# Performance work log

Measured on AMD Instinct MI355X. Metric: run time of the kernel, lower is better.

The kernel has to match this reference:

```python
import jax, jax.numpy as jnp
import numpy as np

H = 16  # n_heads
EPS = 1e-12  # F.normalize eps


def _l2norm(x):
    n = jnp.sqrt(jnp.sum(x * x, axis=-1, keepdims=True))
    return x / jnp.maximum(n, EPS)


def setup_inputs() -> dict:
    key = jax.random.key(0)
    ks = jax.random.split(key, 10)
    bs, S, dim = 2, 2048, 2048
    dh = dim // H
    x = jax.random.normal(ks[0], (bs, S, dim), dtype=jnp.float32)
    mask = jnp.ones((bs, S, S), dtype=jnp.int32)  # mask==0 would be masked out
    s = 0.02
    Wq = jax.random.normal(ks[1], (dim, dim), jnp.float32) * s
    bq = jax.random.normal(ks[2], (dim,), jnp.float32) * s
    Wk = jax.random.normal(ks[3], (dim, dim), jnp.float32) * s
    bk = jax.random.normal(ks[4], (dim,), jnp.float32) * s
    Wv = jax.random.normal(ks[5], (dim, dim), jnp.float32) * s
    bv = jax.random.normal(ks[6], (dim,), jnp.float32) * s
    Wo = jax.random.normal(ks[7], (dim, dim), jnp.float32) * s
    bo = jax.random.normal(ks[8], (dim,), jnp.float32) * s
    attention_scale = jnp.asarray(1.0 / np.sqrt(dh), dtype=jnp.float32)
    return {"x": x, "mask": mask, "Wq": Wq, "bq": bq, "Wk": Wk, "bk": bk,
            "Wv": Wv, "bv": bv, "Wo": Wo, "bo": bo,
            "attention_scale": attention_scale}


def reference(x, mask, Wq, bq, Wk, bk, Wv, bv, Wo, bo, attention_scale):
    bs, S, dim = x.shape
    dh = dim // H

    def split_heads(t):  # [bs,S,dim] -> [bs,H,S,dh]
        return t.reshape(bs, S, H, dh).transpose(0, 2, 1, 3)

    q = split_heads(x @ Wq.T + bq)
    k = split_heads(x @ Wk.T + bk)
    v = split_heads(x @ Wv.T + bv)

    # normalized attention: L2-normalize q,k then learned scale on q
    q = _l2norm(q) * attention_scale
    k = _l2norm(k)

    scores = jnp.einsum('bhqd,bhkd->bhqk', q, k)
    masked = mask[:, None, :, :] == 0  # broadcast over heads
    scores = jnp.where(masked, -jnp.inf, scores)
    weights = jax.nn.softmax(scores.astype(jnp.float32), axis=-1).astype(scores.dtype)
    # dropout p=0.0 -> identity
    ctx = jnp.einsum('bhqk,bhkd->bhqd', weights, v)
    ctx = ctx.transpose(0, 2, 1, 3).reshape(bs, S, dim)
    return ctx @ Wo.T + bo
```

## Files before the change

kernel.cpp:

```cpp
#include <hip/hip_runtime.h>
#include <stdint.h>

typedef __attribute__((ext_vector_type(8))) short short8;
typedef __attribute__((ext_vector_type(4))) float f32x4;
typedef __attribute__((ext_vector_type(4))) unsigned short ushort4v;
typedef __attribute__((ext_vector_type(4))) float float4v;
typedef __attribute__((ext_vector_type(4))) int int4v;

#define GLL16(gp, lp)                                                        \
  __builtin_amdgcn_global_load_lds(                                          \
      (const __attribute__((address_space(1))) void*)(gp),                   \
      (__attribute__((address_space(3))) void*)(lp), 16, 0, 0)

__device__ __forceinline__ unsigned short f2bf(float f) {
  union { float f; unsigned u; } v; v.f = f;
  unsigned r = v.u + 0x7FFFu + ((v.u >> 16) & 1u);
  return (unsigned short)(r >> 16);
}
__device__ __forceinline__ float bf2f(unsigned short h) {
  union { unsigned u; float f; } v; v.u = ((unsigned)h) << 16;
  return v.f;
}

__global__ __launch_bounds__(256) void cast_kernel(
    const float* __restrict__ x, const float* __restrict__ Wq,
    const float* __restrict__ Wk, const float* __restrict__ Wv,
    const float* __restrict__ Wo, const float* __restrict__ bq,
    const float* __restrict__ bk, const float* __restrict__ bv,
    unsigned short* __restrict__ xb, unsigned short* __restrict__ wqkv,
    unsigned short* __restrict__ wob, float* __restrict__ biasq) {
  const int X4 = 2097152, W4 = 1048576;
  const int total = X4 + 4 * W4 + 1536;
  for (int i = blockIdx.x * 256 + threadIdx.x; i < total; i += gridDim.x * 256) {
    if (i < X4 + 4 * W4) {
      const float* src; unsigned short* dst;
      if (i < X4) { src = x + (size_t)i * 4; dst = xb + (size_t)i * 4; }
      else {
        int j = i - X4;
        if (j < 3 * W4) {
          const float* w = (j < W4) ? Wq : (j < 2 * W4 ? Wk : Wv);
          int j0 = (j < W4) ? j : (j < 2 * W4 ? j - W4 : j - 2 * W4);
          src = w + (size_t)j0 * 4; dst = wqkv + (size_t)j * 4;
        } else {
          int j0 = j - 3 * W4; src = Wo + (size_t)j0 * 4; dst = wob + (size_t)j0 * 4;
        }
      }
      float4v v = *(const float4v*)src;
      ushort4v o; o.x = f2bf(v.x); o.y = f2bf(v.y); o.z = f2bf(v.z); o.w = f2bf(v.w);
      *(ushort4v*)dst = o;
    } else {
      int j = i - (X4 + 4 * W4);
      const float* src = (j < 512) ? bq + j * 4
                        : (j < 1024 ? bk + (j - 512) * 4 : bv + (j - 1024) * 4);
      *(float4v*)(biasq + j * 4) = *(const float4v*)src;
    }
  }
}

__global__ __launch_bounds__(256) void maskflag_kernel(const int* __restrict__ mask,
                                                       int* __restrict__ flags) {
  const int bid = blockIdx.x;
  const int b = bid >> 10, rem = bid & 1023, qt = rem >> 5, kt = rem & 31;
  const int t = threadIdx.x;
  const int* mb = mask + (size_t)b * 4194304;
  int ok = 1;
#pragma unroll
  for (int j = 0; j < 4; ++j) {
    int flat = t * 16 + j * 4;
    int r = flat >> 6, c = flat & 63;
    int4v v = *(const int4v*)(mb + (size_t)(qt * 64 + r) * 2048 + kt * 64 + c);
    ok &= (v.x != 0) & (v.y != 0) & (v.z != 0) & (v.w != 0);
  }
  int all = __syncthreads_and(ok);
  if (t == 0) flags[bid] = all;
}

template <bool OUT_BF16>
__global__ __launch_bounds__(256) void gemm_bt(
    const unsigned short* __restrict__ A, const unsigned short* __restrict__ B,
    void* __restrict__ C, const float* __restrict__ bias, int N, int K) {
  __shared__ unsigned short As[128 * 64];
  __shared__ unsigned short Bs[128 * 64];
  const int tid = threadIdx.x, lane = tid & 63;
  const int wid = __builtin_amdgcn_readfirstlane(tid >> 6);
  const int wr = wid >> 1, wc = wid & 1;
  const int bm = blockIdx.y, bn = blockIdx.x;
  const int g = lane >> 4, q15 = lane & 15;
  f32x4 acc[4][4];
#pragma unroll
  for (int i = 0; i < 4; ++i)
#pragma unroll
    for (int j = 0; j < 4; ++j) acc[i][j] = f32x4{0.f, 0.f, 0.f, 0.f};
  const size_t ldab = (size_t)K * 2;
  const int nkt = K >> 6;
  for (int kt = 0; kt < nkt; ++kt) {
#pragma unroll
    for (int i = 0; i < 4; ++i) {
      int c = i * 4 + wid;
      int o = c * 1024 + lane * 16;
      int row = o >> 7, colb = o & 127;
      GLL16((const char*)A + (size_t)(bm * 128 + row) * ldab + kt * 128 + colb,
            (char*)As + c * 1024);
      GLL16((const char*)B + (size_t)(bn * 128 + row) * ldab + kt * 128 + colb,
            (char*)Bs + c * 1024);
    }
    __syncthreads();
#pragma unroll
    for (int kk = 0; kk < 2; ++kk) {
      short8 af[4], bfv[4];
#pragma unroll
      for (int mf = 0; mf < 4; ++mf)
        af[mf] = *(const short8*)((const char*)As +
                 (wr * 64 + mf * 16 + q15) * 128 + kk * 64 + g * 16);
#pragma unroll
      for (int nf = 0; nf < 4; ++nf)
        bfv[nf] = *(const short8*)((const char*)Bs +
                  (wc * 64 + nf * 16 + q15) * 128 + kk * 64 + g * 16);
#pragma unroll
      for (int mf = 0; mf < 4; ++mf)
#pragma unroll
        for (int nf = 0; nf < 4; ++nf)
          acc[mf][nf] = __builtin_amdgcn_mfma_f32_16x16x32_bf16(
              af[mf], bfv[nf], acc[mf][nf], 0, 0, 0);
    }
    __syncthreads();
  }
#pragma unroll
  for (int nf = 0; nf < 4; ++nf) {
    int col = bn * 128 + wc * 64 + nf * 16 + q15;
    float bv = bias[col];
#pragma unroll
    for (int mf = 0; mf < 4; ++mf) {
#pragma unroll
      for (int r = 0; r < 4; ++r) {
        int row = bm * 128 + wr * 64 + mf * 16 + g * 4 + r;
        float v = acc[mf][nf][r] + bv;
        if (OUT_BF16)
          ((unsigned short*)C)[(size_t)row * N + col] = f2bf(v);
        else
          ((float*)C)[(size_t)row * N + col] = v;
      }
    }
  }
}

__global__ __launch_bounds__(256) void norm_vt_kernel(
    unsigned short* __restrict__ QKV, unsigned short* __restrict__ VT,
    const float* __restrict__ scale_p) {
  __shared__ unsigned short vt[128 * 72];
  const int bid = blockIdx.x;
  const int b = bid >> 9, h = (bid >> 5) & 15, st = bid & 31;
  const int t = threadIdx.x;
  const int r = t >> 2, qd = t & 3;
  const float scale = scale_p[0];
  unsigned short* rowp = QKV + (size_t)(b * 2048 + st * 64 + r) * 6144;
#pragma unroll
  for (int part = 0; part < 2; ++part) {
    unsigned short* p = rowp + part * 2048 + h * 128 + qd * 32;
    short8 v[4];
    float ss = 0.f;
#pragma unroll
    for (int j = 0; j < 4; ++j) {
      v[j] = *(const short8*)(p + j * 8);
#pragma unroll
      for (int e = 0; e < 8; ++e) {
        float f = bf2f((unsigned short)v[j][e]);
        ss += f * f;
      }
    }
    ss += __shfl_xor(ss, 1, 64);
    ss += __shfl_xor(ss, 2, 64);
    float inv = 1.0f / fmaxf(sqrtf(ss), 1e-12f);
    if (part == 0) inv *= scale;
#pragma unroll
    for (int j = 0; j < 4; ++j) {
      short8 w;
#pragma unroll
      for (int e = 0; e < 8; ++e)
        w[e] = (short)f2bf(bf2f((unsigned short)v[j][e]) * inv);
      *(short8*)(p + j * 8) = w;
    }
  }
  {
    const unsigned short* p = rowp + 4096 + h * 128 + qd * 32;
#pragma unroll
    for (int j = 0; j < 4; ++j) {
      short8 v = *(const short8*)(p + j * 8);
#pragma unroll
      for (int e = 0; e < 8; ++e) {
        int d = qd * 32 + j * 8 + e;
        vt[d * 72 + r] = (unsigned short)v[e];
      }
    }
  }
  __syncthreads();
  {
    const int d = t >> 1, half = t & 1;
    unsigned short* dst = VT + ((size_t)(b * 16 + h) * 128 + d) * 2048 + st * 64 + half * 32;
#pragma unroll
    for (int j = 0; j < 4; ++j)
      *(short8*)(dst + j * 8) = *(const short8*)(&vt[d * 72 + half * 32 + j * 8]);
  }
}

__global__ __launch_bounds__(256) void flash_kernel(
    const unsigned short* __restrict__ QKV, const unsigned short* __restrict__ VT,
    const int* __restrict__ flags, const int* __restrict__ mask,
    unsigned short* __restrict__ ctx) {
  __shared__ unsigned short Ks[64 * 128];
  __shared__ unsigned short Vs[128 * 64];
  __shared__ unsigned short Ps[4 * 16 * 64];
  const int tid = threadIdx.x, lane = tid & 63;
  const int wid = __builtin_amdgcn_readfirstlane(tid >> 6);
  const int g = lane >> 4, q15 = lane & 15;
  const int bid = blockIdx.x;
  const int b = bid >> 9, h = (bid >> 5) & 15, qt = bid & 31;

  short8 qf[4];
  {
    const char* qbase = (const char*)QKV +
        (size_t)(b * 2048 + qt * 64 + wid * 16 + q15) * 12288 + h * 256;
#pragma unroll
    for (int kk = 0; kk < 4; ++kk)
      qf[kk] = *(const short8*)(qbase + kk * 64 + g * 16);
  }
  f32x4 o[8];
#pragma unroll
  for (int i = 0; i < 8; ++i) o[i] = f32x4{0.f, 0.f, 0.f, 0.f};
  float mrun[4] = {-__builtin_inff(), -__builtin_inff(), -__builtin_inff(), -__builtin_inff()};
  float lrun[4] = {0.f, 0.f, 0.f, 0.f};
  char* PsW = (char*)Ps + wid * 2048;

  for (int kt = 0; kt < 32; ++kt) {
#pragma unroll
    for (int i = 0; i < 8; ++i) {
      int c = i * 4 + wid;
      if (c < 16) {
        int off = c * 1024 + lane * 16;
        int row = off >> 8, colb = off & 255;
        int scol = colb ^ ((row & 7) << 4);
        GLL16((const char*)QKV + (size_t)(b * 2048 + kt * 64 + row) * 12288 +
                  4096 + h * 256 + scol,
              (char*)Ks + c * 1024);
      } else {
        int c2 = c - 16;
        int off = c2 * 1024 + lane * 16;
        int d = off >> 7, colb = off & 127;
        int scol = colb ^ ((d & 7) << 4);
        GLL16((const char*)VT + ((size_t)(b * 16 + h) * 128 + d) * 4096 +
                  kt * 128 + scol,
              (char*)Vs + c2 * 1024);
      }
    }
    __syncthreads();

    f32x4 s[4];
#pragma unroll
    for (int nf = 0; nf < 4; ++nf) s[nf] = f32x4{0.f, 0.f, 0.f, 0.f};
#pragma unroll
    for (int nf = 0; nf < 4; ++nf) {
      int key = nf * 16 + q15;
      const char* kb = (const char*)Ks + key * 256;
      int sw = (key & 7) << 4;
#pragma unroll
      for (int kk = 0; kk < 4; ++kk) {
        short8 kf = *(const short8*)(kb + ((kk * 64 + g * 16) ^ sw));
        s[nf] = __builtin_amdgcn_mfma_f32_16x16x32_bf16(qf[kk], kf, s[nf], 0, 0, 0);
      }
    }

    if (flags[b * 1024 + qt * 32 + kt] == 0) {
#pragma unroll
      for (int nf = 0; nf < 4; ++nf)
#pragma unroll
        for (int r = 0; r < 4; ++r) {
          int q = qt * 64 + wid * 16 + g * 4 + r;
          int k = kt * 64 + nf * 16 + q15;
          if (mask[(size_t)b * 4194304 + (size_t)q * 2048 + k] == 0)
            s[nf][r] = -__builtin_inff();
        }
    }

    float rmax[4];
#pragma unroll
    for (int r = 0; r < 4; ++r)
      rmax[r] = fmaxf(fmaxf(s[0][r], s[1][r]), fmaxf(s[2][r], s[3][r]));
#pragma unroll
    for (int st = 1; st < 16; st <<= 1)
#pragma unroll
      for (int r = 0; r < 4; ++r)
        rmax[r] = fmaxf(rmax[r], __shfl_xor(rmax[r], st, 64));
    float sc_[4];
#pragma unroll
    for (int r = 0; r < 4; ++r) {
      float mn = fmaxf(mrun[r], rmax[r]);
      sc_[r] = __expf(mrun[r] - mn);
      mrun[r] = mn;
      lrun[r] *= sc_[r];
    }
#pragma unroll
    for (int d0 = 0; d0 < 8; ++d0)
#pragma unroll
      for (int r = 0; r < 4; ++r) o[d0][r] *= sc_[r];
    float rs[4] = {0.f, 0.f, 0.f, 0.f};
#pragma unroll
    for (int nf = 0; nf < 4; ++nf)
#pragma unroll
      for (int r = 0; r < 4; ++r) {
        float p = __expf(s[nf][r] - mrun[r]);
        s[nf][r] = p;
        rs[r] += p;
      }
#pragma unroll
    for (int st = 1; st < 16; st <<= 1)
#pragma unroll
      for (int r = 0; r < 4; ++r) rs[r] += __shfl_xor(rs[r], st, 64);
#pragma unroll
    for (int r = 0; r < 4; ++r) lrun[r] += rs[r];

#pragma unroll
    for (int nf = 0; nf < 4; ++nf)
#pragma unroll
      for (int r = 0; r < 4; ++r) {
        int qq = g * 4 + r;
        int kcol = nf * 16 + q15;
        int addr = qq * 128 + ((2 * kcol) ^ ((g & 3) << 4));
        *(unsigned short*)(PsW + addr) = f2bf(s[nf][r]);
      }

#pragma unroll
    for (int kk2 = 0; kk2 < 2; ++kk2) {
      short8 pf = *(const short8*)(PsW + q15 * 128 +
                   ((kk2 * 64 + g * 16) ^ (((q15 >> 2) & 3) << 4)));
#pragma unroll
      for (int d0 = 0; d0 < 8; ++d0) {
        int d = d0 * 16 + q15;
        short8 vf = *(const short8*)((const char*)Vs + d * 128 +
                     ((kk2 * 64 + g * 16) ^ ((d & 7) << 4)));
        o[d0] = __builtin_amdgcn_mfma_f32_16x16x32_bf16(pf, vf, o[d0], 0, 0, 0);
      }
    }
    __syncthreads();
  }

  float inv[4];
#pragma unroll
  for (int r = 0; r < 4; ++r) inv[r] = 1.0f / lrun[r];
#pragma unroll
  for (int d0 = 0; d0 < 8; ++d0)
#pragma unroll
    for (int r = 0; r < 4; ++r) {
      int row = b * 2048 + qt * 64 + wid * 16 + g * 4 + r;
      int col = h * 128 + d0 * 16 + q15;
      ctx[(size_t)row * 2048 + col] = f2bf(o[d0][r] * inv[r]);
    }
}

extern "C" void kernel_launch(void* const* d_in, const int* in_sizes, int n_in,
                              void* d_out, int out_size, void* d_ws, size_t ws_size,
                              hipStream_t stream) {
  const float* x  = (const float*)d_in[0];
  const int* mask = (const int*)d_in[1];
  const float* Wq = (const float*)d_in[2];
  const float* bq = (const float*)d_in[3];
  const float* Wk = (const float*)d_in[4];
  const float* bk = (const float*)d_in[5];
  const float* Wv = (const float*)d_in[6];
  const float* bv = (const float*)d_in[7];
  const float* Wo = (const float*)d_in[8];
  const float* bo = (const float*)d_in[9];
  const float* asc = (const float*)d_in[10];

  char* ws = (char*)d_ws;
  unsigned short* xb   = (unsigned short*)(ws);
  unsigned short* wqkv = (unsigned short*)(ws + ((size_t)16 << 20));
  unsigned short* wob  = (unsigned short*)(ws + ((size_t)40 << 20));
  float* biasq         = (float*)(ws + ((size_t)48 << 20));
  int* flags           = (int*)(ws + ((size_t)48 << 20) + (64 << 10));
  unsigned short* qkv  = (unsigned short*)(ws + ((size_t)49 << 20));
  unsigned short* VT   = wqkv;
  unsigned short* ctx  = xb;
  float* out = (float*)d_out;

  hipLaunchKernelGGL(cast_kernel, dim3(2048), dim3(256), 0, stream,
                     x, Wq, Wk, Wv, Wo, bq, bk, bv, xb, wqkv, wob, biasq);
  hipLaunchKernelGGL(maskflag_kernel, dim3(2048), dim3(256), 0, stream, mask, flags);
  hipLaunchKernelGGL((gemm_bt<true>), dim3(48, 32), dim3(256), 0, stream,
                     xb, wqkv, (void*)qkv, biasq, 6144, 2048);
  hipLaunchKernelGGL(norm_vt_kernel, dim3(1024), dim3(256), 0, stream, qkv, VT, asc);
  hipLaunchKernelGGL(flash_kernel, dim3(1024), dim3(256), 0, stream,
                     qkv, VT, flags, mask, ctx);
  hipLaunchKernelGGL((gemm_bt<false>), dim3(16, 32), dim3(256), 0, stream,
                     ctx, wob, (void*)out, bo, 2048, 2048);
}
```

Before: 552.4 us.

## Restructure flash attention with double-buffered loads, transposed MFMA and lazy rescale

The flash kernel now uses 512-thread blocks covering 128 query rows and double-buffers the K/V tiles in LDS, so the next tile's loads overlap compute on the current one. QK^T is computed transposed, which puts each query row's scores in one lane; the P operand is then built with register shuffles instead of an LDS round trip, and the max and sum reductions shrink to two shuffles. Softmax switches to exp2, with log2(e) folded into the q scale, and the rescale runs only when some row's max grows by more than a threshold. Mask flags are coarsened to 128-row tiles and preloaded as a bitmask, and the output is staged through LDS so the global stores are coalesced. The cost is higher register and LDS pressure, and the lazy rescale relies on the bounded score range of normalized attention.

Result: faster. 490.5 us (-11.2%).

```diff
diff --git a/kernel.cpp b/kernel.cpp
--- a/kernel.cpp
+++ b/kernel.cpp
@@ -1,4 +1,5 @@
 #include <hip/hip_runtime.h>
+#include <hip/hip_bf16.h>
 #include <stdint.h>
 
 typedef __attribute__((ext_vector_type(8))) short short8;
@@ -20,6 +21,11 @@
 __device__ __forceinline__ float bf2f(unsigned short h) {
   union { unsigned u; float f; } v; v.u = ((unsigned)h) << 16;
   return v.f;
+}
+__device__ __forceinline__ unsigned pkbf(float a, float b) {
+  union { __hip_bfloat162 h; unsigned u; } v;
+  v.h = __float22bfloat162_rn(make_float2(a, b));
+  return v.u;
 }
 
 __global__ __launch_bounds__(256) void cast_kernel(
@@ -60,15 +66,15 @@
 __global__ __launch_bounds__(256) void maskflag_kernel(const int* __restrict__ mask,
                                                        int* __restrict__ flags) {
   const int bid = blockIdx.x;
-  const int b = bid >> 10, rem = bid & 1023, qt = rem >> 5, kt = rem & 31;
+  const int b = bid >> 9, qt = (bid >> 5) & 15, kt = bid & 31;
   const int t = threadIdx.x;
   const int* mb = mask + (size_t)b * 4194304;
   int ok = 1;
 #pragma unroll
-  for (int j = 0; j < 4; ++j) {
-    int flat = t * 16 + j * 4;
+  for (int j = 0; j < 8; ++j) {
+    int flat = t * 32 + j * 4;
     int r = flat >> 6, c = flat & 63;
-    int4v v = *(const int4v*)(mb + (size_t)(qt * 64 + r) * 2048 + kt * 64 + c);
+    int4v v = *(const int4v*)(mb + (size_t)(qt * 128 + r) * 2048 + kt * 64 + c);
     ok &= (v.x != 0) & (v.y != 0) & (v.z != 0) & (v.w != 0);
   }
   int all = __syncthreads_and(ok);
@@ -152,7 +158,7 @@
   const int b = bid >> 9, h = (bid >> 5) & 15, st = bid & 31;
   const int t = threadIdx.x;
   const int r = t >> 2, qd = t & 3;
-  const float scale = scale_p[0];
+  const float scale = scale_p[0] * 1.4426950408889634f;
   unsigned short* rowp = QKV + (size_t)(b * 2048 + st * 64 + r) * 6144;
 #pragma unroll
   for (int part = 0; part < 2; ++part) {
@@ -203,157 +209,184 @@
   }
 }
 
-__global__ __launch_bounds__(256) void flash_kernel(
+__global__ __launch_bounds__(512, 4) void flash_kernel(
     const unsigned short* __restrict__ QKV, const unsigned short* __restrict__ VT,
     const int* __restrict__ flags, const int* __restrict__ mask,
     unsigned short* __restrict__ ctx) {
-  __shared__ unsigned short Ks[64 * 128];
-  __shared__ unsigned short Vs[128 * 64];
-  __shared__ unsigned short Ps[4 * 16 * 64];
+  __shared__ char lds[65536];
   const int tid = threadIdx.x, lane = tid & 63;
   const int wid = __builtin_amdgcn_readfirstlane(tid >> 6);
   const int g = lane >> 4, q15 = lane & 15;
   const int bid = blockIdx.x;
-  const int b = bid >> 9, h = (bid >> 5) & 15, qt = bid & 31;
+  const int b = bid >> 8, h = (bid >> 4) & 15, qt = bid & 15;
+
+  unsigned fb = 0;
+#pragma unroll 1
+  for (int i = 0; i < 32; ++i)
+    fb |= (unsigned)(flags[b * 512 + qt * 32 + i] != 0) << i;
 
   short8 qf[4];
   {
     const char* qbase = (const char*)QKV +
-        (size_t)(b * 2048 + qt * 64 + wid * 16 + q15) * 12288 + h * 256;
+        (size_t)(b * 2048 + qt * 128 + wid * 16 + q15) * 12288 + h * 256;
 #pragma unroll
     for (int kk = 0; kk < 4; ++kk)
       qf[kk] = *(const short8*)(qbase + kk * 64 + g * 16);
   }
+
+  const char* sptr;
+  size_t sbase[4]; int ldso[4]; size_t kstep;
+  if (wid < 4) {
+    sptr = (const char*)QKV; kstep = (size_t)64 * 12288;
+#pragma unroll
+    for (int i = 0; i < 4; ++i) {
+      int c = wid * 4 + i;
+      int row = c * 4 + g;
+      int scol = ((lane & 15) * 16) ^ ((row & 7) << 4);
+      sbase[i] = (size_t)(b * 2048 + row) * 12288 + 4096 + h * 256 + scol;
+      ldso[i] = c * 1024;
+    }
+  } else {
+    sptr = (const char*)VT; kstep = 128;
+#pragma unroll
+    for (int i = 0; i < 4; ++i) {
+      int c2 = (wid - 4) * 4 + i;
+      int d = c2 * 8 + (lane >> 3);
+      int scol = ((lane & 7) * 16) ^ ((d & 7) << 4);
+      sbase[i] = ((size_t)((b * 16 + h) * 128 + d)) * 4096 + scol;
+      ldso[i] = 16384 + c2 * 1024;
+    }
+  }
+
   f32x4 o[8];
 #pragma unroll
   for (int i = 0; i < 8; ++i) o[i] = f32x4{0.f, 0.f, 0.f, 0.f};
-  float mrun[4] = {-__builtin_inff(), -__builtin_inff(), -__builtin_inff(), -__builtin_inff()};
-  float lrun[4] = {0.f, 0.f, 0.f, 0.f};
-  char* PsW = (char*)Ps + wid * 2048;
+  float mrun = -1e30f, lrun = 0.f;
+  const int l0 = q15 + 16 * ((2 * g) & 3), l1 = l0 + 16;
+  const bool hi = ((g >> 1) & 1) != 0;
+
+#pragma unroll
+  for (int i = 0; i < 4; ++i) GLL16(sptr + sbase[i], lds + ldso[i]);
+  __syncthreads();
 
   for (int kt = 0; kt < 32; ++kt) {
-#pragma unroll
-    for (int i = 0; i < 8; ++i) {
-      int c = i * 4 + wid;
-      if (c < 16) {
-        int off = c * 1024 + lane * 16;
-        int row = off >> 8, colb = off & 255;
-        int scol = colb ^ ((row & 7) << 4);
-        GLL16((const char*)QKV + (size_t)(b * 2048 + kt * 64 + row) * 12288 +
-                  4096 + h * 256 + scol,
-              (char*)Ks + c * 1024);
-      } else {
-        int c2 = c - 16;
-        int off = c2 * 1024 + lane * 16;
-        int d = off >> 7, colb = off & 127;
-        int scol = colb ^ ((d & 7) << 4);
-        GLL16((const char*)VT + ((size_t)(b * 16 + h) * 128 + d) * 4096 +
-                  kt * 128 + scol,
-              (char*)Vs + c2 * 1024);
-      }
-    }
-    __syncthreads();
+    const int cur = kt & 1;
+    if (kt < 31) {
+#pragma unroll
+      for (int i = 0; i < 4; ++i)
+        GLL16(sptr + sbase[i] + (size_t)(kt + 1) * kstep,
+              lds + (cur ^ 1) * 32768 + ldso[i]);
+    }
+    const char* Ks = lds + cur * 32768;
+    const char* Vs = Ks + 16384;
 
     f32x4 s[4];
 #pragma unroll
     for (int nf = 0; nf < 4; ++nf) s[nf] = f32x4{0.f, 0.f, 0.f, 0.f};
 #pragma unroll
     for (int nf = 0; nf < 4; ++nf) {
-      int key = nf * 16 + q15;
-      const char* kb = (const char*)Ks + key * 256;
-      int sw = (key & 7) << 4;
+      const char* kb = Ks + (nf * 16 + q15) * 256;
+      const int sw = (q15 & 7) << 4;
 #pragma unroll
       for (int kk = 0; kk < 4; ++kk) {
         short8 kf = *(const short8*)(kb + ((kk * 64 + g * 16) ^ sw));
-        s[nf] = __builtin_amdgcn_mfma_f32_16x16x32_bf16(qf[kk], kf, s[nf], 0, 0, 0);
-      }
-    }
-
-    if (flags[b * 1024 + qt * 32 + kt] == 0) {
+        s[nf] = __builtin_amdgcn_mfma_f32_16x16x32_bf16(kf, qf[kk], s[nf], 0, 0, 0);
+      }
+    }
+
+    if (!((fb >> kt) & 1)) {
 #pragma unroll
       for (int nf = 0; nf < 4; ++nf)
 #pragma unroll
         for (int r = 0; r < 4; ++r) {
-          int q = qt * 64 + wid * 16 + g * 4 + r;
-          int k = kt * 64 + nf * 16 + q15;
-          if (mask[(size_t)b * 4194304 + (size_t)q * 2048 + k] == 0)
+          int key = kt * 64 + nf * 16 + g * 4 + r;
+          int q = qt * 128 + wid * 16 + q15;
+          if (mask[(size_t)b * 4194304 + (size_t)q * 2048 + key] == 0)
             s[nf][r] = -__builtin_inff();
         }
     }
 
-    float rmax[4];
-#pragma unroll
-    for (int r = 0; r < 4; ++r)
-      rmax[r] = fmaxf(fmaxf(s[0][r], s[1][r]), fmaxf(s[2][r], s[3][r]));
-#pragma unroll
-    for (int st = 1; st < 16; st <<= 1)
-#pragma unroll
-      for (int r = 0; r < 4; ++r)
-        rmax[r] = fmaxf(rmax[r], __shfl_xor(rmax[r], st, 64));
-    float sc_[4];
-#pragma unroll
-    for (int r = 0; r < 4; ++r) {
-      float mn = fmaxf(mrun[r], rmax[r]);
-      sc_[r] = __expf(mrun[r] - mn);
-      mrun[r] = mn;
-      lrun[r] *= sc_[r];
-    }
-#pragma unroll
-    for (int d0 = 0; d0 < 8; ++d0)
-#pragma unroll
-      for (int r = 0; r < 4; ++r) o[d0][r] *= sc_[r];
-    float rs[4] = {0.f, 0.f, 0.f, 0.f};
+    float pmax = s[0][0];
 #pragma unroll
     for (int nf = 0; nf < 4; ++nf)
 #pragma unroll
+      for (int r = 0; r < 4; ++r) pmax = fmaxf(pmax, s[nf][r]);
+    pmax = fmaxf(pmax, __shfl_xor(pmax, 16, 64));
+    pmax = fmaxf(pmax, __shfl_xor(pmax, 32, 64));
+
+    if (__any(pmax - mrun > 8.0f)) {
+      float mnew = fmaxf(mrun, pmax);
+      float sc = exp2f(mrun - mnew);
+      mrun = mnew; lrun *= sc;
+#pragma unroll
+      for (int d0 = 0; d0 < 8; ++d0)
+#pragma unroll
+        for (int r = 0; r < 4; ++r) o[d0][r] *= sc;
+    }
+
+    float rs = 0.f;
+#pragma unroll
+    for (int nf = 0; nf < 4; ++nf)
+#pragma unroll
       for (int r = 0; r < 4; ++r) {
-        float p = __expf(s[nf][r] - mrun[r]);
-        s[nf][r] = p;
-        rs[r] += p;
-      }
-#pragma unroll
-    for (int st = 1; st < 16; st <<= 1)
-#pragma unroll
-      for (int r = 0; r < 4; ++r) rs[r] += __shfl_xor(rs[r], st, 64);
-#pragma unroll
-    for (int r = 0; r < 4; ++r) lrun[r] += rs[r];
-
-#pragma unroll
-    for (int nf = 0; nf < 4; ++nf)
-#pragma unroll
-      for (int r = 0; r < 4; ++r) {
-        int qq = g * 4 + r;
-        int kcol = nf * 16 + q15;
-        int addr = qq * 128 + ((2 * kcol) ^ ((g & 3) << 4));
-        *(unsigned short*)(PsW + addr) = f2bf(s[nf][r]);
-      }
+        float p = exp2f(s[nf][r] - mrun);
+        s[nf][r] = p; rs += p;
+      }
+    rs += __shfl_xor(rs, 16, 64);
+    rs += __shfl_xor(rs, 32, 64);
+    lrun += rs;
+
+    unsigned pk[4][2];
+#pragma unroll
+    for (int nf = 0; nf < 4; ++nf) {
+      pk[nf][0] = pkbf(s[nf][0], s[nf][1]);
+      pk[nf][1] = pkbf(s[nf][2], s[nf][3]);
+    }
 
 #pragma unroll
     for (int kk2 = 0; kk2 < 2; ++kk2) {
-      short8 pf = *(const short8*)(PsW + q15 * 128 +
-                   ((kk2 * 64 + g * 16) ^ (((q15 >> 2) & 3) << 4)));
+      unsigned w0a = __shfl(pk[2*kk2][0], l0, 64), w0b = __shfl(pk[2*kk2+1][0], l0, 64);
+      unsigned w1a = __shfl(pk[2*kk2][1], l0, 64), w1b = __shfl(pk[2*kk2+1][1], l0, 64);
+      unsigned w2a = __shfl(pk[2*kk2][0], l1, 64), w2b = __shfl(pk[2*kk2+1][0], l1, 64);
+      unsigned w3a = __shfl(pk[2*kk2][1], l1, 64), w3b = __shfl(pk[2*kk2+1][1], l1, 64);
+      union { unsigned u[4]; short8 s8; } pu;
+      pu.u[0] = hi ? w0b : w0a;
+      pu.u[1] = hi ? w1b : w1a;
+      pu.u[2] = hi ? w2b : w2a;
+      pu.u[3] = hi ? w3b : w3a;
 #pragma unroll
       for (int d0 = 0; d0 < 8; ++d0) {
         int d = d0 * 16 + q15;
-        short8 vf = *(const short8*)((const char*)Vs + d * 128 +
+        short8 vf = *(const short8*)(Vs + d * 128 +
                      ((kk2 * 64 + g * 16) ^ ((d & 7) << 4)));
-        o[d0] = __builtin_amdgcn_mfma_f32_16x16x32_bf16(pf, vf, o[d0], 0, 0, 0);
+        o[d0] = __builtin_amdgcn_mfma_f32_16x16x32_bf16(vf, pu.s8, o[d0], 0, 0, 0);
       }
     }
     __syncthreads();
   }
 
-  float inv[4];
-#pragma unroll
-  for (int r = 0; r < 4; ++r) inv[r] = 1.0f / lrun[r];
-#pragma unroll
-  for (int d0 = 0; d0 < 8; ++d0)
-#pragma unroll
-    for (int r = 0; r < 4; ++r) {
-      int row = b * 2048 + qt * 64 + wid * 16 + g * 4 + r;
-      int col = h * 128 + d0 * 16 + q15;
-      ctx[(size_t)row * 2048 + col] = f2bf(o[d0][r] * inv[r]);
-    }
+  float invl = 1.0f / lrun;
+  {
+    char* ost = lds;
+    int rb = (wid * 16 + q15) * 256;
+    int sw = (q15 & 7) << 4;
+#pragma unroll
+    for (int d0 = 0; d0 < 8; ++d0)
+#pragma unroll
+      for (int j = 0; j < 2; ++j) {
+        unsigned w = pkbf(o[d0][2 * j] * invl, o[d0][2 * j + 1] * invl);
+        *(unsigned*)(ost + rb + ((d0 * 32 + g * 8 + j * 4) ^ sw)) = w;
+      }
+  }
+  __syncthreads();
+#pragma unroll
+  for (int p = 0; p < 4; ++p) {
+    int flat = p * 512 + tid;
+    int row = flat >> 4, c16 = flat & 15;
+    short8 v = *(const short8*)(lds + row * 256 + ((c16 * 16) ^ ((row & 7) << 4)));
+    *(short8*)((char*)ctx + (size_t)(b * 2048 + qt * 128 + row) * 4096 +
+               h * 256 + c16 * 16) = v;
+  }
 }
 
 extern "C" void kernel_launch(void* const* d_in, const int* in_sizes, int n_in,
@@ -384,11 +417,11 @@
 
   hipLaunchKernelGGL(cast_kernel, dim3(2048), dim3(256), 0, stream,
                      x, Wq, Wk, Wv, Wo, bq, bk, bv, xb, wqkv, wob, biasq);
-  hipLaunchKernelGGL(maskflag_kernel, dim3(2048), dim3(256), 0, stream, mask, flags);
+  hipLaunchKernelGGL(maskflag_kernel, dim3(1024), dim3(256), 0, stream, mask, flags);
   hipLaunchKernelGGL((gemm_bt<true>), dim3(48, 32), dim3(256), 0, stream,
                      xb, wqkv, (void*)qkv, biasq, 6144, 2048);
   hipLaunchKernelGGL(norm_vt_kernel, dim3(1024), dim3(256), 0, stream, qkv, VT, asc);
-  hipLaunchKernelGGL(flash_kernel, dim3(1024), dim3(256), 0, stream,
+  hipLaunchKernelGGL(flash_kernel, dim3(512), dim3(512), 0, stream,
                      qkv, VT, flags, mask, ctx);
   hipLaunchKernelGGL((gemm_bt<false>), dim3(16, 32), dim3(256), 0, stream,
                      ctx, wob, (void*)out, bo, 2048, 2048);
```
